# Optimization experiments

Hardware: AMD Instinct MI355X
Metric: run time of the kernel (lower is better)

Reference implementation:

```python
import jax, jax.numpy as jnp
import numpy as np

NUM_GRAPHS = 512
LEAKY_SLOPE = 0.01


def _gconv(x, src, dst, w, W_root, W_rel, b_rel):
    # PyG GraphConv: out = lin_rel(sum_j w_ij * x_j) + lin_root(x)
    msg = x[src] * w[:, None]                       # [E, d] gather + scale
    agg = jax.ops.segment_sum(msg, dst, num_segments=x.shape[0])  # scatter-add
    return agg @ W_rel + b_rel + x @ W_root


def setup_inputs() -> dict:
    key = jax.random.key(0)
    ks = jax.random.split(key, 12)
    N, E, D, H, C = 100000, 1250000, 64, 64, 8
    x_embeddings = jax.random.normal(ks[0], (N, D), dtype=jnp.float32)
    edge_index = jax.random.randint(ks[1], (2, E), 0, N, dtype=jnp.int64)
    weights = jax.random.uniform(ks[2], (E,), dtype=jnp.float32)
    batch = jnp.sort(jax.random.randint(ks[3], (N,), 0, NUM_GRAPHS, dtype=jnp.int64))
    s1 = 1.0 / np.sqrt(D)
    s2 = 1.0 / np.sqrt(H)
    W1_root = jax.random.uniform(ks[4], (D, H), jnp.float32, -s1, s1)
    W1_rel = jax.random.uniform(ks[5], (D, H), jnp.float32, -s1, s1)
    b1 = jax.random.uniform(ks[6], (H,), jnp.float32, -s1, s1)
    W2_root = jax.random.uniform(ks[7], (H, H), jnp.float32, -s2, s2)
    W2_rel = jax.random.uniform(ks[8], (H, H), jnp.float32, -s2, s2)
    b2 = jax.random.uniform(ks[9], (H,), jnp.float32, -s2, s2)
    Wl_root = jax.random.uniform(ks[10], (H, C), jnp.float32, -s2, s2)
    bl = jax.random.uniform(ks[11], (C,), jnp.float32, -s2, s2)
    return {"x_embeddings": x_embeddings, "edge_index": edge_index,
            "weights": weights, "batch": batch,
            "W1_root": W1_root, "W1_rel": W1_rel, "b1": b1,
            "W2_root": W2_root, "W2_rel": W2_rel, "b2": b2,
            "Wl_root": Wl_root, "bl": bl}


def reference(x_embeddings, edge_index, weights, batch,
              W1_root, W1_rel, b1, W2_root, W2_rel, b2, Wl_root, bl):
    src, dst = edge_index[0], edge_index[1]
    x = _gconv(x_embeddings, src, dst, weights, W1_root, W1_rel, b1)
    x = jax.nn.leaky_relu(x, LEAKY_SLOPE)
    x = _gconv(x, src, dst, weights, W2_root, W2_rel, b2)
    x = jax.nn.leaky_relu(x, LEAKY_SLOPE)
    # global_mean_pool over graph ids
    summed = jax.ops.segment_sum(x, batch, num_segments=NUM_GRAPHS)
    counts = jax.ops.segment_sum(jnp.ones((x.shape[0],), x.dtype), batch,
                                 num_segments=NUM_GRAPHS)
    pooled = summed / jnp.maximum(counts, 1.0)[:, None]
    # final GraphConv applied with no edges: agg = 0 -> W_root x + b_rel
    out = pooled @ Wl_root + bl
    return out
```

## Files before the change

### kernel.cpp

```cpp
#include <hip/hip_runtime.h>

#define LEAKY_SLOPE 0.01f
#define NUM_GRAPHS 512
#define TILE 4096
#define NB_MAX 512
#define POOL_SPAN 8

typedef __attribute__((ext_vector_type(8))) short short8;
typedef __attribute__((ext_vector_type(4))) float f32x4;

static __device__ __forceinline__ unsigned short f2bf(float f) {
    unsigned u = __float_as_uint(f);
    u += 0x7FFFu + ((u >> 16) & 1u);
    return (unsigned short)(u >> 16);
}
static __device__ __forceinline__ float bf2f(unsigned short h) {
    return __uint_as_float(((unsigned)h) << 16);
}

static __device__ __forceinline__ int wave_incl_scan(int v, int lane) {
#pragma unroll
    for (int off = 1; off < 64; off <<= 1) {
        int t = __shfl_up(v, off, 64);
        if (lane >= off) v += t;
    }
    return v;
}

__global__ __launch_bounds__(256)
void mega_prep(const int* __restrict__ dst, int* __restrict__ bucketCnt, int E,
               int NB, int histBlocks,
               const float* __restrict__ x, unsigned short* __restrict__ xB,
               int xElems , int xBlocks,
               const float* __restrict__ W1rel, const float* __restrict__ W1root,
               const float* __restrict__ W2rel, const float* __restrict__ W2root,
               unsigned short* __restrict__ Bt1, unsigned short* __restrict__ Bt2) {
    const int bid = blockIdx.x;
    if (bid < histBlocks) {
        __shared__ int h[NB_MAX];
        for (int t = threadIdx.x; t < NB_MAX; t += 256) h[t] = 0;
        __syncthreads();
        const int base = bid * TILE;
#pragma unroll
        for (int i = 0; i < TILE / 256; ++i) {
            int e = base + i * 256 + threadIdx.x;
            if (e < E) atomicAdd(&h[dst[e] >> 8], 1);
        }
        __syncthreads();
        for (int t = threadIdx.x; t < NB; t += 256)
            if (h[t]) atomicAdd(&bucketCnt[t], h[t]);
    } else if (bid < histBlocks + xBlocks) {
        int i = (bid - histBlocks) * 256 + threadIdx.x;
        if (i < xElems) {
            float4 f = ((const float4*)x)[i];
            ushort4 o = make_ushort4(f2bf(f.x), f2bf(f.y), f2bf(f.z), f2bf(f.w));
            ((ushort4*)xB)[i] = o;
        }
    } else {
        int b2 = bid - histBlocks - xBlocks;
        for (int idx = b2 * 2048 + threadIdx.x; idx < (b2 + 1) * 2048; idx += 256) {
            int which = idx >> 13;
            int j = idx & 8191;
            int n = j >> 7, k = j & 127;
            const float* Wr = which ? W2rel : W1rel;
            const float* Wo = which ? W2root : W1root;
            float v = (k < 64) ? Wr[k * 64 + n] : Wo[(k - 64) * 64 + n];
            (which ? Bt2 : Bt1)[j] = f2bf(v);
        }
    }
}

__global__ __launch_bounds__(512)
void bscan_kernel(const int* __restrict__ bucketCnt, int* __restrict__ bucketBase,
                  int* __restrict__ cursor, int* __restrict__ rowStart,
                  float* __restrict__ pooled, int N, int E, int NB) {
    __shared__ int ws[8];
    const int t = threadIdx.x, lane = t & 63, wid = t >> 6;
    int v = (t < NB) ? bucketCnt[t] : 0;
    int s = wave_incl_scan(v, lane);
    if (lane == 63) ws[wid] = s;
    __syncthreads();
    int add = 0;
    for (int i = 0; i < wid; ++i) add += ws[i];
    if (t < NB) {
        int excl = s + add - v;
        bucketBase[t] = excl;
        cursor[t] = excl;
    }
    if (t == 0) rowStart[N] = E;
    float4 z = make_float4(0.f, 0.f, 0.f, 0.f);
#pragma unroll
    for (int i = 0; i < 16; ++i)
        ((float4*)pooled)[t * 16 + i] = z;
}

__global__ __launch_bounds__(256)
void p1b_partition(const int* __restrict__ src, const int* __restrict__ dst,
                   const float* __restrict__ w, int* __restrict__ cursor,
                   int2* __restrict__ tmp, int E, int NB) {
    __shared__ int h[NB_MAX];
    __shared__ int cur[NB_MAX];
    __shared__ int lstart[NB_MAX];
    __shared__ int gbase[NB_MAX];
    __shared__ int ws[4];
    __shared__ int2 pay[TILE];
    __shared__ unsigned short bk[TILE];

    for (int t = threadIdx.x; t < NB_MAX; t += 256) h[t] = 0;
    __syncthreads();

    const int base = blockIdx.x * TILE;
    int   myb[TILE / 256];
    int   myp[TILE / 256];
    float myw[TILE / 256];
#pragma unroll
    for (int i = 0; i < TILE / 256; ++i) {
        int e = base + i * 256 + threadIdx.x;
        if (e < E) {
            int d = dst[e];
            myb[i] = d >> 8;
            myp[i] = src[e] | ((d & 255) << 20);
            myw[i] = w[e];
            atomicAdd(&h[myb[i]], 1);
        } else {
            myb[i] = -1;
        }
    }
    __syncthreads();

    {
        const int t = threadIdx.x, lane = t & 63, wid = t >> 6;
        int a = h[2 * t], b = h[2 * t + 1];
        int s = wave_incl_scan(a + b, lane);
        if (lane == 63) ws[wid] = s;
        __syncthreads();
        int add = 0;
        for (int i = 0; i < wid; ++i) add += ws[i];
        int excl = s + add - (a + b);
        lstart[2 * t] = excl;
        lstart[2 * t + 1] = excl + a;
        cur[2 * t] = excl;
        cur[2 * t + 1] = excl + a;
    }
    __syncthreads();

#pragma unroll
    for (int i = 0; i < TILE / 256; ++i) {
        if (myb[i] >= 0) {
            int p = atomicAdd(&cur[myb[i]], 1);
            pay[p] = make_int2(myp[i], __float_as_int(myw[i]));
            bk[p] = (unsigned short)myb[i];
        }
    }
    __syncthreads();

    for (int t = threadIdx.x; t < NB; t += 256) {
        int c = h[t];
        if (c) gbase[t] = atomicAdd(&cursor[t], c);
    }
    __syncthreads();

    const int total = min(TILE, E - base);
    for (int s2 = threadIdx.x; s2 < total; s2 += 256) {
        int b2 = bk[s2];
        tmp[gbase[b2] + s2 - lstart[b2]] = pay[s2];
    }
}

__global__ __launch_bounds__(256)
void p2_build(const int2* __restrict__ tmp, const int* __restrict__ bucketBase,
              int* __restrict__ rowStart, int2* __restrict__ edata,
              int N, int E, int NB) {
    const int b = blockIdx.x;
    const int s = bucketBase[b];
    const int e2 = (b + 1 < NB) ? bucketBase[b + 1] : E;
    __shared__ int h[256];
    __shared__ int cur[256];
    __shared__ int ws[4];
    h[threadIdx.x] = 0;
    __syncthreads();
    for (int j = s + threadIdx.x; j < e2; j += 256) {
        int dl = (tmp[j].x >> 20) & 255;
        atomicAdd(&h[dl], 1);
    }
    __syncthreads();
    const int t = threadIdx.x, lane = t & 63, wid = t >> 6;
    int v = h[t];
    int sc = wave_incl_scan(v, lane);
    if (lane == 63) ws[wid] = sc;
    __syncthreads();
    int add = 0;
    for (int i = 0; i < wid; ++i) add += ws[i];
    int excl = sc + add - v;
    const int node = b * 256 + t;
    if (node < N) rowStart[node] = s + excl;
    cur[t] = excl;
    __syncthreads();
    for (int j = s + threadIdx.x; j < e2; j += 256) {
        int2 v2 = tmp[j];
        int dl = (v2.x >> 20) & 255;
        int p = atomicAdd(&cur[dl], 1);
        edata[s + p] = make_int2(v2.x & 0x1FFFF, v2.y);
    }
}

template <int POOL>
__global__ __launch_bounds__(256)
void fused_layer(const unsigned short* __restrict__ xin,
                 const int* __restrict__ rowStart,
                 const int2* __restrict__ edata,
                 const unsigned short* __restrict__ Bt,
                 const float* __restrict__ bias,
                 unsigned short* __restrict__ xoutB,
                 const int* __restrict__ batch,
                 float* __restrict__ pooled, int N) {
    const int lane = threadIdx.x & 63;
    const int wave = threadIdx.x >> 6;
    const int grp  = lane >> 4;
    const int l16  = lane & 15;
    const int f4   = l16 * 4;
    const int m0   = (int)blockIdx.x * 128 + wave * 32;

    __shared__ __align__(16) unsigned short aggL[4][32][72];
    __shared__ float lpool[POOL_SPAN * 64];

    int gmin = 0;
    if (POOL) {
        int b0 = (int)blockIdx.x * 128;
        gmin = batch[b0 < N ? b0 : N - 1];
        for (int i = threadIdx.x; i < POOL_SPAN * 64; i += 256) lpool[i] = 0.f;
    }

    int rsv = 0;
    if (lane <= 32) {
        int rn = m0 + lane;
        rsv = rowStart[rn < N ? rn : N];
    }
#pragma unroll 1
    for (int i = 0; i < 32; ++i) {
        const int s = __shfl(rsv, i, 64);
        const int e = __shfl(rsv, i + 1, 64);
        float a0 = 0.f, a1 = 0.f, a2 = 0.f, a3 = 0.f;
        for (int j = s; j < e; j += 16) {
            int2 ed[4];
#pragma unroll
            for (int u = 0; u < 4; ++u) {
                int ii = j + u * 4 + grp;
                ed[u] = edata[ii < e ? ii : s];
            }
            ushort4 r[4];
#pragma unroll
            for (int u = 0; u < 4; ++u)
                r[u] = *(const ushort4*)(xin + (size_t)ed[u].x * 64 + f4);
#pragma unroll
            for (int u = 0; u < 4; ++u) {
                float wv = (j + u * 4 + grp < e) ? __int_as_float(ed[u].y) : 0.0f;
                a0 += bf2f(r[u].x) * wv;  a1 += bf2f(r[u].y) * wv;
                a2 += bf2f(r[u].z) * wv;  a3 += bf2f(r[u].w) * wv;
            }
        }
        a0 += __shfl_xor(a0, 16, 64);  a1 += __shfl_xor(a1, 16, 64);
        a2 += __shfl_xor(a2, 16, 64);  a3 += __shfl_xor(a3, 16, 64);
        a0 += __shfl_xor(a0, 32, 64);  a1 += __shfl_xor(a1, 32, 64);
        a2 += __shfl_xor(a2, 32, 64);  a3 += __shfl_xor(a3, 32, 64);
        if (grp == 0)
            *(ushort4*)(&aggL[wave][i][f4]) =
                make_ushort4(f2bf(a0), f2bf(a1), f2bf(a2), f2bf(a3));
    }

    short8 bf[4][4];
#pragma unroll
    for (int t = 0; t < 4; ++t)
#pragma unroll
        for (int k = 0; k < 4; ++k)
            bf[t][k] = *(const short8*)(Bt + (t * 16 + l16) * 128 + k * 32 + grp * 8);

    f32x4 acc[2][4];
#pragma unroll
    for (int s = 0; s < 2; ++s)
#pragma unroll
        for (int t = 0; t < 4; ++t)
            acc[s][t] = (f32x4){0.f, 0.f, 0.f, 0.f};

#pragma unroll
    for (int s = 0; s < 2; ++s) {
        int row = m0 + s * 16 + l16;
        int rowc = row < N ? row : N - 1;
        const unsigned short* xrow = xin + (size_t)rowc * 64;
        short8 af[4];
        af[0] = *(const short8*)(&aggL[wave][s * 16 + l16][grp * 8]);
        af[1] = *(const short8*)(&aggL[wave][s * 16 + l16][32 + grp * 8]);
        af[2] = *(const short8*)(xrow + grp * 8);
        af[3] = *(const short8*)(xrow + 32 + grp * 8);
#pragma unroll
        for (int t = 0; t < 4; ++t)
#pragma unroll
            for (int k = 0; k < 4; ++k) {
                if (POOL == 0)
                    acc[s][t] = __builtin_amdgcn_mfma_f32_16x16x32_bf16(
                        bf[t][k], af[k], acc[s][t], 0, 0, 0);
                else
                    acc[s][t] = __builtin_amdgcn_mfma_f32_16x16x32_bf16(
                        af[k], bf[t][k], acc[s][t], 0, 0, 0);
            }
    }

    if (POOL == 0) {
#pragma unroll
        for (int s = 0; s < 2; ++s) {
            const int node = m0 + s * 16 + l16;
            if (node < N) {
#pragma unroll
                for (int t = 0; t < 4; ++t) {
                    const float4 bb = *(const float4*)(bias + t * 16 + grp * 4);
                    float v0 = acc[s][t][0] + bb.x;
                    float v1 = acc[s][t][1] + bb.y;
                    float v2 = acc[s][t][2] + bb.z;
                    float v3 = acc[s][t][3] + bb.w;
                    v0 = (v0 > 0.f) ? v0 : LEAKY_SLOPE * v0;
                    v1 = (v1 > 0.f) ? v1 : LEAKY_SLOPE * v1;
                    v2 = (v2 > 0.f) ? v2 : LEAKY_SLOPE * v2;
                    v3 = (v3 > 0.f) ? v3 : LEAKY_SLOPE * v3;
                    ushort4 o = make_ushort4(f2bf(v0), f2bf(v1), f2bf(v2), f2bf(v3));
                    *(ushort4*)(xoutB + (size_t)node * 64 + t * 16 + grp * 4) = o;
                }
            }
        }
    } else {
        __syncthreads();
#pragma unroll
        for (int s = 0; s < 2; ++s) {
#pragma unroll
            for (int t = 0; t < 4; ++t) {
                const int col = t * 16 + l16;
                const float b = bias[col];
                const int rowbase = m0 + s * 16 + grp * 4;
                float v[4]; int g[4]; int nv = 0;
#pragma unroll
                for (int r = 0; r < 4; ++r) {
                    int row = rowbase + r;
                    if (row < N) {
                        float a = acc[s][t][r] + b;
                        a = (a > 0.0f) ? a : LEAKY_SLOPE * a;
                        v[nv] = a;
                        g[nv] = batch[row];
                        ++nv;
                    }
                }
                if (nv == 4 && g[0] == g[3]) {
                    int gl = g[0] - gmin;
                    float sum = v[0] + v[1] + v[2] + v[3];
                    if (gl < POOL_SPAN) atomicAdd(&lpool[gl * 64 + col], sum);
                    else                atomicAdd(&pooled[g[0] * 64 + col], sum);
                } else {
                    for (int r = 0; r < nv; ++r) {
                        int gl = g[r] - gmin;
                        if (gl < POOL_SPAN) atomicAdd(&lpool[gl * 64 + col], v[r]);
                        else                atomicAdd(&pooled[g[r] * 64 + col], v[r]);
                    }
                }
            }
        }
        __syncthreads();
        for (int i = threadIdx.x; i < POOL_SPAN * 64; i += 256) {
            float vv = lpool[i];
            if (vv != 0.0f)
                atomicAdd(&pooled[(gmin + (i >> 6)) * 64 + (i & 63)], vv);
        }
    }
}

__global__ __launch_bounds__(64)
void final_kernel(const float* __restrict__ pooled, const int* __restrict__ batch,
                  int N, const float* __restrict__ Wl, const float* __restrict__ bl,
                  float* __restrict__ out) {
    const int g = blockIdx.x;
    const int j = threadIdx.x;
    __shared__ float sp[64];
    __shared__ int scnt;
    if (j == 0) {
        int lo = 0, hi = N;
        while (lo < hi) { int mid = (lo + hi) >> 1; if (batch[mid] < g) lo = mid + 1; else hi = mid; }
        const int start = lo;
        hi = N;
        while (lo < hi) { int mid = (lo + hi) >> 1; if (batch[mid] < g + 1) lo = mid + 1; else hi = mid; }
        scnt = lo - start;
    }
    __syncthreads();
    const float c = fmaxf((float)scnt, 1.0f);
    sp[j] = pooled[g * 64 + j] / c;
    __syncthreads();
    if (j < 8) {
        float acc = bl[j];
#pragma unroll
        for (int k = 0; k < 64; ++k) acc += sp[k] * Wl[k * 8 + j];
        out[g * 8 + j] = acc;
    }
}

extern "C" void kernel_launch(void* const* d_in, const int* in_sizes, int n_in,
                              void* d_out, int out_size, void* d_ws, size_t ws_size,
                              hipStream_t stream) {
    const float* x      = (const float*)d_in[0];
    const int*   ei     = (const int*)  d_in[1];
    const float* w      = (const float*)d_in[2];
    const int*   batch  = (const int*)  d_in[3];
    const float* W1root = (const float*)d_in[4];
    const float* W1rel  = (const float*)d_in[5];
    const float* b1     = (const float*)d_in[6];
    const float* W2root = (const float*)d_in[7];
    const float* W2rel  = (const float*)d_in[8];
    const float* b2     = (const float*)d_in[9];
    const float* Wl     = (const float*)d_in[10];
    const float* bl     = (const float*)d_in[11];
    float* out = (float*)d_out;

    const int E = in_sizes[2];
    const int N = in_sizes[3];
    const int* src = ei;
    const int* dst = ei + E;
    const int NB = (N + 255) / 256;

    unsigned short* xB   = (unsigned short*)d_ws;
    unsigned short* aggB = xB   + (size_t)N * 64;
    unsigned short* x1B  = aggB + (size_t)N * 64;
    int2*  tmp      = (int2*)(x1B + (size_t)N * 64);
    int2*  edata    = tmp + E;
    unsigned short* Bt1 = (unsigned short*)(edata + E);
    unsigned short* Bt2 = Bt1 + 64 * 128;
    int*   rowStart = (int*)(Bt2 + 64 * 128);
    int*   bucketCnt  = rowStart + (N + 1);
    int*   bucketBase = bucketCnt + NB_MAX;
    int*   cursor     = bucketBase + NB_MAX;
    float* pooled   = (float*)(cursor + NB_MAX);
    (void)aggB;

    const int histBlocks = (E + TILE - 1) / TILE;
    const int xElems = N * 16;
    const int xBlocks = (xElems + 255) / 256;

    (void)hipMemsetAsync(bucketCnt, 0, NB_MAX * sizeof(int), stream);
    mega_prep<<<histBlocks + xBlocks + 8, 256, 0, stream>>>(
        dst, bucketCnt, E, NB, histBlocks,
        x, xB, xElems, xBlocks,
        W1rel, W1root, W2rel, W2root, Bt1, Bt2);
    bscan_kernel<<<1, 512, 0, stream>>>(bucketCnt, bucketBase, cursor, rowStart,
                                        pooled, N, E, NB);
    p1b_partition<<<histBlocks, 256, 0, stream>>>(src, dst, w, cursor, tmp, E, NB);
    p2_build<<<NB, 256, 0, stream>>>(tmp, bucketBase, rowStart, edata, N, E, NB);

    const int tBlocks = (N + 127) / 128;
    fused_layer<0><<<tBlocks, 256, 0, stream>>>(xB, rowStart, edata, Bt1, b1,
                                                x1B, nullptr, nullptr, N);
    fused_layer<1><<<tBlocks, 256, 0, stream>>>(x1B, rowStart, edata, Bt2, b2,
                                                nullptr, batch, pooled, N);
    final_kernel<<<NUM_GRAPHS, 64, 0, stream>>>(pooled, batch, N, Wl, bl, out);
}
```

Before: 292.3 us.

## Shrink fused layer block to 32 nodes, split gather across waves

```diff
diff --git a/kernel.cpp b/kernel.cpp
--- a/kernel.cpp
+++ b/kernel.cpp
@@ -219,15 +219,14 @@
     const int grp  = lane >> 4;
     const int l16  = lane & 15;
     const int f4   = l16 * 4;
-    const int m0   = (int)blockIdx.x * 128 + wave * 32;
-
-    __shared__ __align__(16) unsigned short aggL[4][32][72];
+    const int m0   = (int)blockIdx.x * 32;
+
+    __shared__ __align__(16) unsigned short aggL[32][72];
     __shared__ float lpool[POOL_SPAN * 64];
 
     int gmin = 0;
     if (POOL) {
-        int b0 = (int)blockIdx.x * 128;
-        gmin = batch[b0 < N ? b0 : N - 1];
+        gmin = batch[m0 < N ? m0 : N - 1];
         for (int i = threadIdx.x; i < POOL_SPAN * 64; i += 256) lpool[i] = 0.f;
     }
 
@@ -237,7 +236,8 @@
         rsv = rowStart[rn < N ? rn : N];
     }
 #pragma unroll 1
-    for (int i = 0; i < 32; ++i) {
+    for (int k = 0; k < 8; ++k) {
+        const int i = wave * 8 + k;
         const int s = __shfl(rsv, i, 64);
         const int e = __shfl(rsv, i + 1, 64);
         float a0 = 0.f, a1 = 0.f, a2 = 0.f, a3 = 0.f;
@@ -264,59 +264,58 @@
         a0 += __shfl_xor(a0, 32, 64);  a1 += __shfl_xor(a1, 32, 64);
         a2 += __shfl_xor(a2, 32, 64);  a3 += __shfl_xor(a3, 32, 64);
         if (grp == 0)
-            *(ushort4*)(&aggL[wave][i][f4]) =
+            *(ushort4*)(&aggL[i][f4]) =
                 make_ushort4(f2bf(a0), f2bf(a1), f2bf(a2), f2bf(a3));
     }
 
-    short8 bf[4][4];
-#pragma unroll
-    for (int t = 0; t < 4; ++t)
-#pragma unroll
-        for (int k = 0; k < 4; ++k)
-            bf[t][k] = *(const short8*)(Bt + (t * 16 + l16) * 128 + k * 32 + grp * 8);
-
-    f32x4 acc[2][4];
-#pragma unroll
-    for (int s = 0; s < 2; ++s)
+    __syncthreads();
+
+    if (wave < 2) {
+        const int s = wave;
+        short8 bf[4][4];
 #pragma unroll
         for (int t = 0; t < 4; ++t)
-            acc[s][t] = (f32x4){0.f, 0.f, 0.f, 0.f};
-
-#pragma unroll
-    for (int s = 0; s < 2; ++s) {
-        int row = m0 + s * 16 + l16;
-        int rowc = row < N ? row : N - 1;
-        const unsigned short* xrow = xin + (size_t)rowc * 64;
-        short8 af[4];
-        af[0] = *(const short8*)(&aggL[wave][s * 16 + l16][grp * 8]);
-        af[1] = *(const short8*)(&aggL[wave][s * 16 + l16][32 + grp * 8]);
-        af[2] = *(const short8*)(xrow + grp * 8);
-        af[3] = *(const short8*)(xrow + 32 + grp * 8);
+#pragma unroll
+            for (int k = 0; k < 4; ++k)
+                bf[t][k] = *(const short8*)(Bt + (t * 16 + l16) * 128 + k * 32 + grp * 8);
+
+        f32x4 acc[4];
 #pragma unroll
         for (int t = 0; t < 4; ++t)
-#pragma unroll
-            for (int k = 0; k < 4; ++k) {
-                if (POOL == 0)
-                    acc[s][t] = __builtin_amdgcn_mfma_f32_16x16x32_bf16(
-                        bf[t][k], af[k], acc[s][t], 0, 0, 0);
-                else
-                    acc[s][t] = __builtin_amdgcn_mfma_f32_16x16x32_bf16(
-                        af[k], bf[t][k], acc[s][t], 0, 0, 0);
-            }
-    }
-
-    if (POOL == 0) {
-#pragma unroll
-        for (int s = 0; s < 2; ++s) {
+            acc[t] = (f32x4){0.f, 0.f, 0.f, 0.f};
+
+        {
+            int row = m0 + s * 16 + l16;
+            int rowc = row < N ? row : N - 1;
+            const unsigned short* xrow = xin + (size_t)rowc * 64;
+            short8 af[4];
+            af[0] = *(const short8*)(&aggL[s * 16 + l16][grp * 8]);
+            af[1] = *(const short8*)(&aggL[s * 16 + l16][32 + grp * 8]);
+            af[2] = *(const short8*)(xrow + grp * 8);
+            af[3] = *(const short8*)(xrow + 32 + grp * 8);
+#pragma unroll
+            for (int t = 0; t < 4; ++t)
+#pragma unroll
+                for (int k = 0; k < 4; ++k) {
+                    if (POOL == 0)
+                        acc[t] = __builtin_amdgcn_mfma_f32_16x16x32_bf16(
+                            bf[t][k], af[k], acc[t], 0, 0, 0);
+                    else
+                        acc[t] = __builtin_amdgcn_mfma_f32_16x16x32_bf16(
+                            af[k], bf[t][k], acc[t], 0, 0, 0);
+                }
+        }
+
+        if (POOL == 0) {
             const int node = m0 + s * 16 + l16;
             if (node < N) {
 #pragma unroll
                 for (int t = 0; t < 4; ++t) {
                     const float4 bb = *(const float4*)(bias + t * 16 + grp * 4);
-                    float v0 = acc[s][t][0] + bb.x;
-                    float v1 = acc[s][t][1] + bb.y;
-                    float v2 = acc[s][t][2] + bb.z;
-                    float v3 = acc[s][t][3] + bb.w;
+                    float v0 = acc[t][0] + bb.x;
+                    float v1 = acc[t][1] + bb.y;
+                    float v2 = acc[t][2] + bb.z;
+                    float v3 = acc[t][3] + bb.w;
                     v0 = (v0 > 0.f) ? v0 : LEAKY_SLOPE * v0;
                     v1 = (v1 > 0.f) ? v1 : LEAKY_SLOPE * v1;
                     v2 = (v2 > 0.f) ? v2 : LEAKY_SLOPE * v2;
@@ -325,11 +324,7 @@
                     *(ushort4*)(xoutB + (size_t)node * 64 + t * 16 + grp * 4) = o;
                 }
             }
-        }
-    } else {
-        __syncthreads();
-#pragma unroll
-        for (int s = 0; s < 2; ++s) {
+        } else {
 #pragma unroll
             for (int t = 0; t < 4; ++t) {
                 const int col = t * 16 + l16;
@@ -340,7 +335,7 @@
                 for (int r = 0; r < 4; ++r) {
                     int row = rowbase + r;
                     if (row < N) {
-                        float a = acc[s][t][r] + b;
+                        float a = acc[t][r] + b;
                         a = (a > 0.0f) ? a : LEAKY_SLOPE * a;
                         v[nv] = a;
                         g[nv] = batch[row];
@@ -361,6 +356,9 @@
                 }
             }
         }
+    }
+
+    if (POOL) {
         __syncthreads();
         for (int i = threadIdx.x; i < POOL_SPAN * 64; i += 256) {
             float vv = lpool[i];
@@ -449,10 +447,10 @@
     p1b_partition<<<histBlocks, 256, 0, stream>>>(src, dst, w, cursor, tmp, E, NB);
     p2_build<<<NB, 256, 0, stream>>>(tmp, bucketBase, rowStart, edata, N, E, NB);
 
-    const int tBlocks = (N + 127) / 128;
-    fused_layer<0><<<tBlocks, 256, 0, stream>>>(xB, rowStart, edata, Bt1, b1,
+    const int fBlocks = (N + 31) / 32;
+    fused_layer<0><<<fBlocks, 256, 0, stream>>>(xB, rowStart, edata, Bt1, b1,
                                                 x1B, nullptr, nullptr, N);
-    fused_layer<1><<<tBlocks, 256, 0, stream>>>(x1B, rowStart, edata, Bt2, b2,
+    fused_layer<1><<<fBlocks, 256, 0, stream>>>(x1B, rowStart, edata, Bt2, b2,
                                                 nullptr, batch, pooled, N);
     final_kernel<<<NUM_GRAPHS, 64, 0, stream>>>(pooled, batch, N, Wl, bl, out);
 }
```

New measurement: 271.2 us. 1.08x faster.
